# Optimization experiments

Hardware: AMD Instinct MI355X
Metric: run time of the kernel (lower is better)

## Reference

```python
import jax, jax.numpy as jnp
import numpy as np

B, S, H, E, C, V = 512, 256, 768, 6, 10, 3


def setup_inputs() -> dict:
    key = jax.random.key(0)
    ks = jax.random.split(key, 16)

    def w(k, shape):
        fan_in = shape[-1]
        return jax.random.normal(k, shape, dtype=jnp.float32) / np.sqrt(fan_in)

    return {
        'x': jax.random.randint(ks[0], (B, S), 0, V, dtype=jnp.int64),
        'emb': w(ks[1], (V, E)),
        'W_fx': w(ks[2], (H, E)), 'W_fh': w(ks[3], (H, H)), 'b_f': w(ks[4], (H, 1)),
        'W_ix': w(ks[5], (H, E)), 'W_ih': w(ks[6], (H, H)), 'b_i': w(ks[7], (H, 1)),
        'W_ox': w(ks[8], (H, E)), 'W_oh': w(ks[9], (H, H)), 'b_o': w(ks[10], (H, 1)),
        'W_cx': w(ks[11], (H, E)), 'b_c': w(ks[12], (H, 1)),
        'W_ph': w(ks[13], (C, H)), 'b_p': w(ks[14], (C, 1)),
        'c_init': jax.random.normal(ks[15], (H, B), dtype=jnp.float32) / np.sqrt(B),
    }


def reference(x, emb, W_fx, W_fh, b_f, W_ix, W_ih, b_i, W_ox, W_oh, b_o,
              W_cx, b_c, W_ph, b_p, c_init):
    # Embed tokens: [B, S] -> [B, S, E] -> time-major [S, E, B]
    xe = jnp.transpose(emb[x], (1, 2, 0))
    xs = xe[: S - 1]  # loop runs seq_length - 1 steps

    def step(carry, x_t):
        c_prev, _ = carry  # c_prev: [H, B], x_t: [E, B]
        f_t = jax.nn.sigmoid(W_fx @ x_t + W_fh @ c_prev + b_f)
        i_t = jax.nn.sigmoid(W_ix @ x_t + W_ih @ c_prev + b_i)
        o_t = jax.nn.sigmoid(W_ox @ x_t + W_oh @ c_prev + b_o)
        c_t = jax.nn.sigmoid(W_cx @ x_t + b_c) * i_t + c_prev * f_t
        h_t = jnp.tanh(c_t) * o_t
        return (c_t, h_t), None

    h0 = jnp.zeros((H, B), dtype=c_init.dtype)
    (c_fin, h_fin), _ = jax.lax.scan(step, (c_init, h0), xs)
    p_t = W_ph @ h_fin + b_p  # [C, B]
    return jax.nn.log_softmax(p_t.T, axis=-1)  # [B, C]
```

## Files before the change

kernel.cpp:

```cpp
#include <hip/hip_runtime.h>


typedef _Float16 f16x8 __attribute__((ext_vector_type(8)));
typedef _Float16 f16x4 __attribute__((ext_vector_type(4)));
typedef float    f32x4 __attribute__((ext_vector_type(4)));

#define Hdim  768
#define Bdim  512
#define Sdim  256
#define NSTEP 255
#define Edim  6
#define NCls  10
#define NGRP  16
#define NRB   12
#define GC    32
#define HB    64
#define NKK   24
#define CSTR  776
#define XSTR  260
#define PLANE (Bdim * Hdim)
#define SCL      4096.0f
#define SCL_INV  2.44140625e-4f

#define WP_FRAGS   (2 * NRB * 4 * NKK * 64)
#define WS_CBUF    0u
#define WS_HFIN    (2u * 2u * PLANE * 2u)
#define WS_BAR     (WS_HFIN + Bdim * Hdim * 4u)
#define WS_WPK     (WS_BAR + 4096u)
#define WS_BAR_BYTES (NGRP * 16u * 4u)

__device__ __forceinline__ float sigf(float z) { return 1.0f / (1.0f + __expf(-z)); }

__device__ __forceinline__ f32x4 mf(f16x8 a, f16x8 b, f32x4 c) {
    return __builtin_amdgcn_mfma_f32_16x16x32_f16(a, b, c, 0, 0, 0);
}

__global__ void __launch_bounds__(256)
prep_w(const float* __restrict__ Wfh, const float* __restrict__ Wih,
       _Float16* __restrict__ wpk)
{
    const int fid  = blockIdx.x * 256 + threadIdx.x;
    const int lane = fid & 63;
    const int t1   = fid >> 6;
    const int kk   = t1 % NKK;
    const int gi   = t1 / NKK;
    const int sub  = gi & 3;
    const int t3   = gi >> 2;
    const int rb   = t3 % NRB;
    const int gate = t3 / NRB;
    const int q = lane >> 4, r = lane & 15;
    const int row = rb * 64 + sub * 16 + r;
    const int col = kk * 32 + q * 8;
    const float* src = (gate ? Wih : Wfh) + (size_t)row * Hdim + col;
    f16x8 hi, lo;
    #pragma unroll
    for (int j = 0; j < 8; ++j) {
        const float v = src[j];
        const _Float16 h = (_Float16)v;
        hi[j] = h;
        lo[j] = (_Float16)((v - (float)h) * SCL);
    }
    *(f16x8*)&wpk[(size_t)fid * 8] = hi;
    *(f16x8*)&wpk[((size_t)WP_FRAGS + fid) * 8] = lo;
}

__global__ void __launch_bounds__(512, 1)
lstm_persist(const int* __restrict__ xk, const float* __restrict__ emb,
             const float* __restrict__ Wfx, const float* __restrict__ bfv,
             const float* __restrict__ Wix, const float* __restrict__ biv,
             const float* __restrict__ Wox, const float* __restrict__ Woh,
             const float* __restrict__ bov,
             const float* __restrict__ Wcx, const float* __restrict__ bcv,
             const float* __restrict__ cinit,
             const _Float16* __restrict__ wpk,
             _Float16* __restrict__ cbuf, float* __restrict__ hfin,
             unsigned int* __restrict__ bar)
{
    __shared__ __align__(16) _Float16 ldsH[GC * CSTR];
    __shared__ __align__(16) _Float16 ldsM[GC * CSTR];
    __shared__ __align__(16) float    tbl[3 * HB * 4];
    __shared__ __align__(16) float    zbuf[HB * GC];
    __shared__ __align__(4)  unsigned char xtok[GC * XSTR];
    __shared__ int s_flag;
    __shared__ unsigned int fdone;

    const int tid  = threadIdx.x;
    const int w    = tid >> 6;
    const int lane = tid & 63;
    const int q    = lane >> 4;
    const int r    = lane & 15;
    const int gt   = w >> 2;
    const int sub  = w & 3;
    const int bid  = blockIdx.x;
    const int g    = bid & 15;
    const int rb   = bid >> 4;
    const int blkh0 = rb * HB;
    const int gc0   = g * GC;
    const int hq0   = blkh0 + sub * 16 + q * 4;
    const int gi    = (gt * NRB + rb) * 4 + sub;

    if (tid == 0) { s_flag = 0; fdone = 0u; }
    __syncthreads();
    if (tid < 256) {
        if (xk[(size_t)gc0 * Sdim + 2 * tid + 1] != 0) s_flag = 1;
    }
    if (tid < 3 * HB) {
        const int v  = tid >> 6;
        const int hl = tid & 63;
        const int hg = blkh0 + hl;
        float pf = bfv[hg], pi = biv[hg], po = bov[hg], pc = bcv[hg];
        #pragma unroll
        for (int e = 0; e < Edim; ++e) {
            const float ev = emb[v * Edim + e];
            pf += Wfx[hg * Edim + e] * ev;
            pi += Wix[hg * Edim + e] * ev;
            po += Wox[hg * Edim + e] * ev;
            pc += Wcx[hg * Edim + e] * ev;
        }
        float* t = &tbl[(v * HB + hl) * 4];
        t[0] = pf; t[1] = pi; t[2] = po; t[3] = sigf(pc);
    }
    __syncthreads();
    const int is64 = (s_flag == 0);

    {
        const int col   = tid >> 4;
        const int sbase = (tid & 15) * 16;
        const size_t rowb = (size_t)(gc0 + col) * Sdim;
        for (int k2 = 0; k2 < 16; ++k2) {
            const int s0 = sbase + k2;
            const size_t idx = rowb + s0;
            xtok[col * XSTR + s0] = (unsigned char)xk[is64 ? (idx << 1) : idx];
        }
    }

    f16x8 whi[NKK], wlo[NKK];
    #pragma unroll
    for (int kk = 0; kk < NKK; ++kk) {
        whi[kk] = *(const f16x8*)&wpk[((size_t)(gi * NKK + kk) * 64 + lane) * 8];
        wlo[kk] = *(const f16x8*)&wpk[((size_t)WP_FRAGS + (size_t)(gi * NKK + kk) * 64 + lane) * 8];
    }

    float cst[2][4];
    #pragma unroll
    for (int ct = 0; ct < 2; ++ct) {
        const int b = gc0 + ct * 16 + r;
        #pragma unroll
        for (int reg = 0; reg < 4; ++reg)
            cst[ct][reg] = cinit[(size_t)(hq0 + reg) * Bdim + b];
    }

    for (int i = 0; i < 48; ++i) {
        const int idx = tid + i * 512;
        const int col = idx & 31, k = idx >> 5;
        const float v = cinit[(size_t)k * Bdim + gc0 + col];
        const _Float16 h = (_Float16)v;
        ldsH[col * CSTR + k] = h;
        ldsM[col * CSTR + k] = (_Float16)((v - (float)h) * SCL);
    }

    for (int s = 0; s < NSTEP; ++s) {
        __syncthreads();

        f32x4 a0h = {0,0,0,0}, a0x = {0,0,0,0}, a1h = {0,0,0,0}, a1x = {0,0,0,0};
        #pragma unroll
        for (int kk = 0; kk < NKK; ++kk) {
            const int lo = kk * 32 + q * 8;
            const f16x8 bh0 = *(const f16x8*)&ldsH[ r       * CSTR + lo];
            const f16x8 bm0 = *(const f16x8*)&ldsM[ r       * CSTR + lo];
            const f16x8 bh1 = *(const f16x8*)&ldsH[(16 + r) * CSTR + lo];
            const f16x8 bm1 = *(const f16x8*)&ldsM[(16 + r) * CSTR + lo];
            a0h = mf(whi[kk], bh0, a0h);
            a0x = mf(whi[kk], bm0, a0x);
            a0x = mf(wlo[kk], bh0, a0x);
            a1h = mf(whi[kk], bh1, a1h);
            a1x = mf(whi[kk], bm1, a1x);
            a1x = mf(wlo[kk], bh1, a1x);
        }
        if (gt) {
            #pragma unroll
            for (int ct = 0; ct < 2; ++ct) {
                const f32x4 zh = ct ? a1h : a0h;
                const f32x4 zx = ct ? a1x : a0x;
                #pragma unroll
                for (int reg = 0; reg < 4; ++reg)
                    zbuf[(sub * 16 + q * 4 + reg) * GC + ct * 16 + r] =
                        zh[reg] + zx[reg] * SCL_INV;
            }
        }
        __syncthreads();

        if (!gt) {
            if (s != NSTEP - 1) {
                _Float16* cwH = cbuf + (size_t)(((s + 1) & 1) * 2) * PLANE;
                _Float16* cwM = cwH + PLANE;
                #pragma unroll
                for (int ct = 0; ct < 2; ++ct) {
                    const int bl = ct * 16 + r;
                    const int v  = xtok[bl * XSTR + s];
                    const float* tb = &tbl[(v * HB + sub * 16 + q * 4) * 4];
                    const f32x4 zh = ct ? a1h : a0h;
                    const f32x4 zx = ct ? a1x : a0x;
                    f16x4 cvh, cvm;
                    #pragma unroll
                    for (int reg = 0; reg < 4; ++reg) {
                        const float zf = zh[reg] + zx[reg] * SCL_INV;
                        const float zi = zbuf[(sub * 16 + q * 4 + reg) * GC + bl];
                        const float* tt = tb + reg * 4;
                        const float fg = sigf(zf + tt[0]);
                        const float ig = sigf(zi + tt[1]);
                        const float cn = tt[3] * ig + cst[ct][reg] * fg;
                        cst[ct][reg] = cn;
                        const _Float16 ch = (_Float16)cn;
                        cvh[reg] = ch;
                        cvm[reg] = (_Float16)((cn - (float)ch) * SCL);
                    }
                    unsigned long long uh, um;
                    __builtin_memcpy(&uh, &cvh, 8);
                    __builtin_memcpy(&um, &cvm, 8);
                    const size_t eo = (size_t)(gc0 + bl) * Hdim + hq0;
                    __hip_atomic_store((unsigned long long*)&cwH[eo], uh,
                                       __ATOMIC_RELAXED, __HIP_MEMORY_SCOPE_AGENT);
                    __hip_atomic_store((unsigned long long*)&cwM[eo], um,
                                       __ATOMIC_RELAXED, __HIP_MEMORY_SCOPE_AGENT);
                }
                asm volatile("s_waitcnt vmcnt(0)" ::: "memory");
                if (lane == 0) {
                    const unsigned old = __hip_atomic_fetch_add(&fdone, 1u,
                                         __ATOMIC_ACQ_REL, __HIP_MEMORY_SCOPE_WORKGROUP);
                    if (old == 4u * (unsigned)s + 3u)
                        __hip_atomic_store(&bar[g * 16 + rb], (unsigned)(s + 1),
                                           __ATOMIC_RELAXED, __HIP_MEMORY_SCOPE_AGENT);
                }
            } else {
                f32x4 o0h = {0,0,0,0}, o0x = {0,0,0,0}, o1h = {0,0,0,0}, o1x = {0,0,0,0};
                const int arow = blkh0 + sub * 16 + r;
                #pragma unroll
                for (int kk = 0; kk < NKK; ++kk) {
                    const float* wp = Woh + (size_t)arow * Hdim + kk * 32 + q * 8;
                    f16x8 who;
                    #pragma unroll
                    for (int j = 0; j < 8; ++j) who[j] = (_Float16)wp[j];
                    const int lo = kk * 32 + q * 8;
                    const f16x8 bh0 = *(const f16x8*)&ldsH[ r       * CSTR + lo];
                    const f16x8 bm0 = *(const f16x8*)&ldsM[ r       * CSTR + lo];
                    const f16x8 bh1 = *(const f16x8*)&ldsH[(16 + r) * CSTR + lo];
                    const f16x8 bm1 = *(const f16x8*)&ldsM[(16 + r) * CSTR + lo];
                    o0h = mf(who, bh0, o0h);  o0x = mf(who, bm0, o0x);
                    o1h = mf(who, bh1, o1h);  o1x = mf(who, bm1, o1x);
                }
                #pragma unroll
                for (int ct = 0; ct < 2; ++ct) {
                    const int bl = ct * 16 + r;
                    const int v  = xtok[bl * XSTR + s];
                    const float* tb = &tbl[(v * HB + sub * 16 + q * 4) * 4];
                    const f32x4 zh = ct ? a1h : a0h;
                    const f32x4 zx = ct ? a1x : a0x;
                    const f32x4 zoh = ct ? o1h : o0h;
                    const f32x4 zox = ct ? o1x : o0x;
                    f32x4 hv;
                    #pragma unroll
                    for (int reg = 0; reg < 4; ++reg) {
                        const float zf = zh[reg] + zx[reg] * SCL_INV;
                        const float zi = zbuf[(sub * 16 + q * 4 + reg) * GC + bl];
                        const float zo = zoh[reg] + zox[reg] * SCL_INV;
                        const float* tt = tb + reg * 4;
                        const float fg = sigf(zf + tt[0]);
                        const float ig = sigf(zi + tt[1]);
                        const float og = sigf(zo + tt[2]);
                        const float cn = tt[3] * ig + cst[ct][reg] * fg;
                        const float e  = __expf(-2.0f * fabsf(cn));
                        const float th = __builtin_copysignf((1.0f - e) / (1.0f + e), cn);
                        hv[reg] = th * og;
                    }
                    *(f32x4*)&hfin[(size_t)(gc0 + bl) * Hdim + hq0] = hv;
                }
            }
        }

        if (s < NSTEP - 1) {
            const unsigned tgt = (unsigned)(s + 1);
            while (true) {
                unsigned vv = tgt;
                if (lane < NRB)
                    vv = __hip_atomic_load(&bar[g * 16 + lane],
                                           __ATOMIC_RELAXED, __HIP_MEMORY_SCOPE_AGENT);
                if (__all(vv >= tgt)) break;
                __builtin_amdgcn_s_sleep(1);
            }
            const _Float16* crH = cbuf + (size_t)(((s + 1) & 1) * 2) * PLANE;
            const _Float16* crM = crH + PLANE;
            const int col = tid >> 4, j = tid & 15;
            const size_t rowo = (size_t)(gc0 + col) * Hdim;
            {
                unsigned long long th[12];
                #pragma unroll
                for (int i = 0; i < 12; ++i)
                    th[i] = __hip_atomic_load((unsigned long long*)&crH[rowo + (j + 16 * i) * 4],
                                              __ATOMIC_RELAXED, __HIP_MEMORY_SCOPE_AGENT);
                #pragma unroll
                for (int i = 0; i < 12; ++i)
                    *(unsigned long long*)&ldsH[col * CSTR + (j + 16 * i) * 4] = th[i];
            }
            {
                unsigned long long tm[12];
                #pragma unroll
                for (int i = 0; i < 12; ++i)
                    tm[i] = __hip_atomic_load((unsigned long long*)&crM[rowo + (j + 16 * i) * 4],
                                              __ATOMIC_RELAXED, __HIP_MEMORY_SCOPE_AGENT);
                #pragma unroll
                for (int i = 0; i < 12; ++i)
                    *(unsigned long long*)&ldsM[col * CSTR + (j + 16 * i) * 4] = tm[i];
            }
        }
    }
}

__global__ void __launch_bounds__(64)
proj_kernel(const float* __restrict__ hfin, const float* __restrict__ Wph,
            const float* __restrict__ bpv, float* __restrict__ out)
{
    const int b = blockIdx.x;
    const int lane = threadIdx.x;
    float acc[NCls];
    #pragma unroll
    for (int c = 0; c < NCls; ++c) acc[c] = 0.f;
    const float* hb = &hfin[(size_t)b * Hdim];
    for (int i = 0; i < Hdim / 64; ++i) {
        const float hv = hb[lane + i * 64];
        #pragma unroll
        for (int c = 0; c < NCls; ++c)
            acc[c] += Wph[c * Hdim + lane + i * 64] * hv;
    }
    #pragma unroll
    for (int c = 0; c < NCls; ++c) {
        float v = acc[c];
        #pragma unroll
        for (int off = 32; off > 0; off >>= 1)
            v += __shfl_xor(v, off, 64);
        acc[c] = v + bpv[c];
    }
    float m = acc[0];
    #pragma unroll
    for (int c = 1; c < NCls; ++c) m = fmaxf(m, acc[c]);
    float ssum = 0.f;
    #pragma unroll
    for (int c = 0; c < NCls; ++c) ssum += __expf(acc[c] - m);
    const float lse = m + __logf(ssum);
    if (lane < NCls) out[b * NCls + lane] = acc[lane] - lse;
}

extern "C" void kernel_launch(void* const* d_in, const int* in_sizes, int n_in,
                              void* d_out, int out_size, void* d_ws, size_t ws_size,
                              hipStream_t stream)
{
    const int*   xk    = (const int*)d_in[0];
    const float* emb   = (const float*)d_in[1];
    const float* Wfx   = (const float*)d_in[2];
    const float* Wfh   = (const float*)d_in[3];
    const float* bfv   = (const float*)d_in[4];
    const float* Wix   = (const float*)d_in[5];
    const float* Wih   = (const float*)d_in[6];
    const float* biv   = (const float*)d_in[7];
    const float* Wox   = (const float*)d_in[8];
    const float* Woh   = (const float*)d_in[9];
    const float* bov   = (const float*)d_in[10];
    const float* Wcx   = (const float*)d_in[11];
    const float* bcv   = (const float*)d_in[12];
    const float* Wph   = (const float*)d_in[13];
    const float* bpv   = (const float*)d_in[14];
    const float* cinit = (const float*)d_in[15];

    char* ws = (char*)d_ws;
    _Float16*     cbuf = (_Float16*)(ws + WS_CBUF);
    float*        hfin = (float*)(ws + WS_HFIN);
    unsigned int* bar  = (unsigned int*)(ws + WS_BAR);
    _Float16*     wpk  = (_Float16*)(ws + WS_WPK);

    hipMemsetAsync(bar, 0, WS_BAR_BYTES, stream);

    prep_w<<<dim3(WP_FRAGS / 256), dim3(256), 0, stream>>>(Wfh, Wih, wpk);

    lstm_persist<<<dim3(NGRP * NRB), dim3(512), 0, stream>>>(
        xk, emb, Wfx, bfv, Wix, biv, Wox, Woh, bov, Wcx, bcv,
        cinit, wpk, cbuf, hfin, bar);

    proj_kernel<<<dim3(Bdim), dim3(64), 0, stream>>>(hfin, Wph, bpv, (float*)d_out);
}
```

Measured before the change: 2.582 ms.

## Add dedicated loader warps with per-chunk LDS flags to overlap state fetch with MFMA

Raises the block to 768 threads so four extra warps become producers. They poll each row-block's global barrier flag on its own and copy that chunk of the fp16 hi/lo state into LDS, then release per-chunk ready counters. The eight compute warps start MFMAs on each K-chunk as soon as it lands, which replaces the block-wide syncthreads and the all-rows barrier wait. zbuf is double-buffered and handed off through an LDS counter. The cost is more spin-waiting on LDS atomics and extra register pressure from the larger block, which keepalive asm is used to pin weights in registers.

```diff
diff --git a/kernel.cpp b/kernel.cpp
--- a/kernel.cpp
+++ b/kernel.cpp
@@ -4,6 +4,7 @@
 typedef _Float16 f16x8 __attribute__((ext_vector_type(8)));
 typedef _Float16 f16x4 __attribute__((ext_vector_type(4)));
 typedef float    f32x4 __attribute__((ext_vector_type(4)));
+typedef unsigned long long u64;
 
 #define Hdim  768
 #define Bdim  512
@@ -16,6 +17,7 @@
 #define GC    32
 #define HB    64
 #define NKK   24
+#define NCH   12
 #define CSTR  776
 #define XSTR  260
 #define PLANE (Bdim * Hdim)
@@ -33,6 +35,10 @@
 
 __device__ __forceinline__ f32x4 mf(f16x8 a, f16x8 b, f32x4 c) {
     return __builtin_amdgcn_mfma_f32_16x16x32_f16(a, b, c, 0, 0, 0);
+}
+
+__device__ __forceinline__ void keepalive(f16x8& x) {
+    asm volatile("" : "+v"(x));
 }
 
 __global__ void __launch_bounds__(256)
@@ -64,7 +70,7 @@
     *(f16x8*)&wpk[((size_t)WP_FRAGS + fid) * 8] = lo;
 }
 
-__global__ void __launch_bounds__(512, 1)
+__global__ void __launch_bounds__(768, 1)
 lstm_persist(const int* __restrict__ xk, const float* __restrict__ emb,
              const float* __restrict__ Wfx, const float* __restrict__ bfv,
              const float* __restrict__ Wix, const float* __restrict__ biv,
@@ -79,27 +85,29 @@
     __shared__ __align__(16) _Float16 ldsH[GC * CSTR];
     __shared__ __align__(16) _Float16 ldsM[GC * CSTR];
     __shared__ __align__(16) float    tbl[3 * HB * 4];
-    __shared__ __align__(16) float    zbuf[HB * GC];
+    __shared__ __align__(16) float    zbuf[2][HB * GC];
     __shared__ __align__(4)  unsigned char xtok[GC * XSTR];
+    __shared__ unsigned int ldsRdy[NCH];
+    __shared__ unsigned int chunkDone[NCH];
+    __shared__ unsigned int zdone, fdone;
     __shared__ int s_flag;
-    __shared__ unsigned int fdone;
 
     const int tid  = threadIdx.x;
     const int w    = tid >> 6;
     const int lane = tid & 63;
     const int q    = lane >> 4;
     const int r    = lane & 15;
-    const int gt   = w >> 2;
-    const int sub  = w & 3;
     const int bid  = blockIdx.x;
     const int g    = bid & 15;
     const int rb   = bid >> 4;
     const int blkh0 = rb * HB;
     const int gc0   = g * GC;
-    const int hq0   = blkh0 + sub * 16 + q * 4;
-    const int gi    = (gt * NRB + rb) * 4 + sub;
-
-    if (tid == 0) { s_flag = 0; fdone = 0u; }
+
+    if (tid == 0) {
+        s_flag = 0; zdone = 0u; fdone = 0u;
+        #pragma unroll
+        for (int j = 0; j < NCH; ++j) { ldsRdy[j] = 0u; chunkDone[j] = 0u; }
+    }
     __syncthreads();
     if (tid < 256) {
         if (xk[(size_t)gc0 * Sdim + 2 * tid + 1] != 0) s_flag = 1;
@@ -123,7 +131,7 @@
     __syncthreads();
     const int is64 = (s_flag == 0);
 
-    {
+    if (tid < 512) {
         const int col   = tid >> 4;
         const int sbase = (tid & 15) * 16;
         const size_t rowb = (size_t)(gc0 + col) * Sdim;
@@ -134,183 +142,209 @@
         }
     }
 
-    f16x8 whi[NKK], wlo[NKK];
-    #pragma unroll
-    for (int kk = 0; kk < NKK; ++kk) {
-        whi[kk] = *(const f16x8*)&wpk[((size_t)(gi * NKK + kk) * 64 + lane) * 8];
-        wlo[kk] = *(const f16x8*)&wpk[((size_t)WP_FRAGS + (size_t)(gi * NKK + kk) * 64 + lane) * 8];
-    }
-
-    float cst[2][4];
-    #pragma unroll
-    for (int ct = 0; ct < 2; ++ct) {
-        const int b = gc0 + ct * 16 + r;
-        #pragma unroll
-        for (int reg = 0; reg < 4; ++reg)
-            cst[ct][reg] = cinit[(size_t)(hq0 + reg) * Bdim + b];
-    }
-
-    for (int i = 0; i < 48; ++i) {
-        const int idx = tid + i * 512;
+    for (int i = 0; i < 32; ++i) {
+        const int idx = tid + i * 768;
         const int col = idx & 31, k = idx >> 5;
         const float v = cinit[(size_t)k * Bdim + gc0 + col];
         const _Float16 h = (_Float16)v;
         ldsH[col * CSTR + k] = h;
         ldsM[col * CSTR + k] = (_Float16)((v - (float)h) * SCL);
     }
-
-    for (int s = 0; s < NSTEP; ++s) {
-        __syncthreads();
-
-        f32x4 a0h = {0,0,0,0}, a0x = {0,0,0,0}, a1h = {0,0,0,0}, a1x = {0,0,0,0};
+    __syncthreads();
+
+    if (w < 8) {
+        const int gt  = w >> 2;
+        const int sub = w & 3;
+        const int hq0 = blkh0 + sub * 16 + q * 4;
+        const int gi  = (gt * NRB + rb) * 4 + sub;
+
+        f16x8 whi[NKK], wlo[NKK];
         #pragma unroll
         for (int kk = 0; kk < NKK; ++kk) {
-            const int lo = kk * 32 + q * 8;
-            const f16x8 bh0 = *(const f16x8*)&ldsH[ r       * CSTR + lo];
-            const f16x8 bm0 = *(const f16x8*)&ldsM[ r       * CSTR + lo];
-            const f16x8 bh1 = *(const f16x8*)&ldsH[(16 + r) * CSTR + lo];
-            const f16x8 bm1 = *(const f16x8*)&ldsM[(16 + r) * CSTR + lo];
-            a0h = mf(whi[kk], bh0, a0h);
-            a0x = mf(whi[kk], bm0, a0x);
-            a0x = mf(wlo[kk], bh0, a0x);
-            a1h = mf(whi[kk], bh1, a1h);
-            a1x = mf(whi[kk], bm1, a1x);
-            a1x = mf(wlo[kk], bh1, a1x);
-        }
-        if (gt) {
+            whi[kk] = *(const f16x8*)&wpk[((size_t)(gi * NKK + kk) * 64 + lane) * 8];
+            wlo[kk] = *(const f16x8*)&wpk[((size_t)WP_FRAGS + (size_t)(gi * NKK + kk) * 64 + lane) * 8];
+        }
+        #pragma unroll
+        for (int kk = 0; kk < NKK; ++kk) { keepalive(whi[kk]); keepalive(wlo[kk]); }
+
+        float cst[2][4];
+        #pragma unroll
+        for (int ct = 0; ct < 2; ++ct) {
+            const int b = gc0 + ct * 16 + r;
             #pragma unroll
-            for (int ct = 0; ct < 2; ++ct) {
-                const f32x4 zh = ct ? a1h : a0h;
-                const f32x4 zx = ct ? a1x : a0x;
+            for (int reg = 0; reg < 4; ++reg)
+                cst[ct][reg] = cinit[(size_t)(hq0 + reg) * Bdim + b];
+        }
+
+        for (int s = 0; s < NSTEP; ++s) {
+            f32x4 a0h = {0,0,0,0}, a0x = {0,0,0,0}, a1h = {0,0,0,0}, a1x = {0,0,0,0};
+            const unsigned rdyTgt = 4u * (unsigned)s;
+            for (int j = 0; j < NCH; ++j) {
+                while (__hip_atomic_load(&ldsRdy[j], __ATOMIC_ACQUIRE,
+                                         __HIP_MEMORY_SCOPE_WORKGROUP) < rdyTgt)
+                    __builtin_amdgcn_s_sleep(1);
                 #pragma unroll
-                for (int reg = 0; reg < 4; ++reg)
-                    zbuf[(sub * 16 + q * 4 + reg) * GC + ct * 16 + r] =
-                        zh[reg] + zx[reg] * SCL_INV;
-            }
-        }
-        __syncthreads();
-
-        if (!gt) {
-            if (s != NSTEP - 1) {
-                _Float16* cwH = cbuf + (size_t)(((s + 1) & 1) * 2) * PLANE;
-                _Float16* cwM = cwH + PLANE;
-                #pragma unroll
-                for (int ct = 0; ct < 2; ++ct) {
-                    const int bl = ct * 16 + r;
-                    const int v  = xtok[bl * XSTR + s];
-                    const float* tb = &tbl[(v * HB + sub * 16 + q * 4) * 4];
-                    const f32x4 zh = ct ? a1h : a0h;
-                    const f32x4 zx = ct ? a1x : a0x;
-                    f16x4 cvh, cvm;
-                    #pragma unroll
-                    for (int reg = 0; reg < 4; ++reg) {
-                        const float zf = zh[reg] + zx[reg] * SCL_INV;
-                        const float zi = zbuf[(sub * 16 + q * 4 + reg) * GC + bl];
-                        const float* tt = tb + reg * 4;
-                        const float fg = sigf(zf + tt[0]);
-                        const float ig = sigf(zi + tt[1]);
-                        const float cn = tt[3] * ig + cst[ct][reg] * fg;
-                        cst[ct][reg] = cn;
-                        const _Float16 ch = (_Float16)cn;
-                        cvh[reg] = ch;
-                        cvm[reg] = (_Float16)((cn - (float)ch) * SCL);
-                    }
-                    unsigned long long uh, um;
-                    __builtin_memcpy(&uh, &cvh, 8);
-                    __builtin_memcpy(&um, &cvm, 8);
-                    const size_t eo = (size_t)(gc0 + bl) * Hdim + hq0;
-                    __hip_atomic_store((unsigned long long*)&cwH[eo], uh,
-                                       __ATOMIC_RELAXED, __HIP_MEMORY_SCOPE_AGENT);
-                    __hip_atomic_store((unsigned long long*)&cwM[eo], um,
-                                       __ATOMIC_RELAXED, __HIP_MEMORY_SCOPE_AGENT);
-                }
-                asm volatile("s_waitcnt vmcnt(0)" ::: "memory");
-                if (lane == 0) {
-                    const unsigned old = __hip_atomic_fetch_add(&fdone, 1u,
-                                         __ATOMIC_ACQ_REL, __HIP_MEMORY_SCOPE_WORKGROUP);
-                    if (old == 4u * (unsigned)s + 3u)
-                        __hip_atomic_store(&bar[g * 16 + rb], (unsigned)(s + 1),
-                                           __ATOMIC_RELAXED, __HIP_MEMORY_SCOPE_AGENT);
-                }
-            } else {
-                f32x4 o0h = {0,0,0,0}, o0x = {0,0,0,0}, o1h = {0,0,0,0}, o1x = {0,0,0,0};
-                const int arow = blkh0 + sub * 16 + r;
-                #pragma unroll
-                for (int kk = 0; kk < NKK; ++kk) {
-                    const float* wp = Woh + (size_t)arow * Hdim + kk * 32 + q * 8;
-                    f16x8 who;
-                    #pragma unroll
-                    for (int j = 0; j < 8; ++j) who[j] = (_Float16)wp[j];
+                for (int k2 = 0; k2 < 2; ++k2) {
+                    const int kk = j * 2 + k2;
                     const int lo = kk * 32 + q * 8;
                     const f16x8 bh0 = *(const f16x8*)&ldsH[ r       * CSTR + lo];
                     const f16x8 bm0 = *(const f16x8*)&ldsM[ r       * CSTR + lo];
                     const f16x8 bh1 = *(const f16x8*)&ldsH[(16 + r) * CSTR + lo];
                     const f16x8 bm1 = *(const f16x8*)&ldsM[(16 + r) * CSTR + lo];
-                    o0h = mf(who, bh0, o0h);  o0x = mf(who, bm0, o0x);
-                    o1h = mf(who, bh1, o1h);  o1x = mf(who, bm1, o1x);
+                    a0h = mf(whi[kk], bh0, a0h);
+                    a0x = mf(whi[kk], bm0, a0x);
+                    a0x = mf(wlo[kk], bh0, a0x);
+                    a1h = mf(whi[kk], bh1, a1h);
+                    a1x = mf(whi[kk], bm1, a1x);
+                    a1x = mf(wlo[kk], bh1, a1x);
                 }
+                if (lane == 0)
+                    __hip_atomic_fetch_add(&chunkDone[j], 1u, __ATOMIC_RELEASE,
+                                           __HIP_MEMORY_SCOPE_WORKGROUP);
+            }
+
+            if (gt) {
+                float* zp = zbuf[s & 1];
                 #pragma unroll
                 for (int ct = 0; ct < 2; ++ct) {
-                    const int bl = ct * 16 + r;
-                    const int v  = xtok[bl * XSTR + s];
-                    const float* tb = &tbl[(v * HB + sub * 16 + q * 4) * 4];
                     const f32x4 zh = ct ? a1h : a0h;
                     const f32x4 zx = ct ? a1x : a0x;
-                    const f32x4 zoh = ct ? o1h : o0h;
-                    const f32x4 zox = ct ? o1x : o0x;
-                    f32x4 hv;
                     #pragma unroll
-                    for (int reg = 0; reg < 4; ++reg) {
-                        const float zf = zh[reg] + zx[reg] * SCL_INV;
-                        const float zi = zbuf[(sub * 16 + q * 4 + reg) * GC + bl];
-                        const float zo = zoh[reg] + zox[reg] * SCL_INV;
-                        const float* tt = tb + reg * 4;
-                        const float fg = sigf(zf + tt[0]);
-                        const float ig = sigf(zi + tt[1]);
-                        const float og = sigf(zo + tt[2]);
-                        const float cn = tt[3] * ig + cst[ct][reg] * fg;
-                        const float e  = __expf(-2.0f * fabsf(cn));
-                        const float th = __builtin_copysignf((1.0f - e) / (1.0f + e), cn);
-                        hv[reg] = th * og;
+                    for (int reg = 0; reg < 4; ++reg)
+                        zp[(sub * 16 + q * 4 + reg) * GC + ct * 16 + r] =
+                            zh[reg] + zx[reg] * SCL_INV;
+                }
+                if (lane == 0)
+                    __hip_atomic_fetch_add(&zdone, 1u, __ATOMIC_RELEASE,
+                                           __HIP_MEMORY_SCOPE_WORKGROUP);
+            } else {
+                const unsigned zTgt = 4u * (unsigned)(s + 1);
+                while (__hip_atomic_load(&zdone, __ATOMIC_ACQUIRE,
+                                         __HIP_MEMORY_SCOPE_WORKGROUP) < zTgt)
+                    __builtin_amdgcn_s_sleep(1);
+                const float* zp = zbuf[s & 1];
+
+                if (s != NSTEP - 1) {
+                    _Float16* cwH = cbuf + (size_t)(((s + 1) & 1) * 2) * PLANE;
+                    _Float16* cwM = cwH + PLANE;
+                    #pragma unroll
+                    for (int ct = 0; ct < 2; ++ct) {
+                        const int bl = ct * 16 + r;
+                        const int v  = xtok[bl * XSTR + s];
+                        const float* tb = &tbl[(v * HB + sub * 16 + q * 4) * 4];
+                        const f32x4 zh = ct ? a1h : a0h;
+                        const f32x4 zx = ct ? a1x : a0x;
+                        f16x4 cvh, cvm;
+                        #pragma unroll
+                        for (int reg = 0; reg < 4; ++reg) {
+                            const float zf = zh[reg] + zx[reg] * SCL_INV;
+                            const float zi = zp[(sub * 16 + q * 4 + reg) * GC + bl];
+                            const float* tt = tb + reg * 4;
+                            const float fg = sigf(zf + tt[0]);
+                            const float ig = sigf(zi + tt[1]);
+                            const float cn = tt[3] * ig + cst[ct][reg] * fg;
+                            cst[ct][reg] = cn;
+                            const _Float16 ch = (_Float16)cn;
+                            cvh[reg] = ch;
+                            cvm[reg] = (_Float16)((cn - (float)ch) * SCL);
+                        }
+                        u64 uh, um;
+                        __builtin_memcpy(&uh, &cvh, 8);
+                        __builtin_memcpy(&um, &cvm, 8);
+                        const size_t eo = (size_t)(gc0 + bl) * Hdim + hq0;
+                        __hip_atomic_store((u64*)&cwH[eo], uh,
+                                           __ATOMIC_RELAXED, __HIP_MEMORY_SCOPE_AGENT);
+                        __hip_atomic_store((u64*)&cwM[eo], um,
+                                           __ATOMIC_RELAXED, __HIP_MEMORY_SCOPE_AGENT);
                     }
-                    *(f32x4*)&hfin[(size_t)(gc0 + bl) * Hdim + hq0] = hv;
+                    asm volatile("s_waitcnt vmcnt(0)" ::: "memory");
+                    if (lane == 0) {
+                        const unsigned old = __hip_atomic_fetch_add(&fdone, 1u,
+                                             __ATOMIC_ACQ_REL, __HIP_MEMORY_SCOPE_WORKGROUP);
+                        if (old == 4u * (unsigned)s + 3u)
+                            __hip_atomic_store(&bar[g * 16 + rb], (unsigned)(s + 1),
+                                               __ATOMIC_RELAXED, __HIP_MEMORY_SCOPE_AGENT);
+                    }
+                } else {
+                    f32x4 o0h = {0,0,0,0}, o0x = {0,0,0,0}, o1h = {0,0,0,0}, o1x = {0,0,0,0};
+                    const int arow = blkh0 + sub * 16 + r;
+                    #pragma unroll
+                    for (int kk = 0; kk < NKK; ++kk) {
+                        const float* wp = Woh + (size_t)arow * Hdim + kk * 32 + q * 8;
+                        f16x8 who;
+                        #pragma unroll
+                        for (int jj = 0; jj < 8; ++jj) who[jj] = (_Float16)wp[jj];
+                        const int lo = kk * 32 + q * 8;
+                        const f16x8 bh0 = *(const f16x8*)&ldsH[ r       * CSTR + lo];
+                        const f16x8 bm0 = *(const f16x8*)&ldsM[ r       * CSTR + lo];
+                        const f16x8 bh1 = *(const f16x8*)&ldsH[(16 + r) * CSTR + lo];
+                        const f16x8 bm1 = *(const f16x8*)&ldsM[(16 + r) * CSTR + lo];
+                        o0h = mf(who, bh0, o0h);  o0x = mf(who, bm0, o0x);
+                        o1h = mf(who, bh1, o1h);  o1x = mf(who, bm1, o1x);
+                    }
+                    #pragma unroll
+                    for (int ct = 0; ct < 2; ++ct) {
+                        const int bl = ct * 16 + r;
+                        const int v  = xtok[bl * XSTR + s];
+                        const float* tb = &tbl[(v * HB + sub * 16 + q * 4) * 4];
+                        const f32x4 zh = ct ? a1h : a0h;
+                        const f32x4 zx = ct ? a1x : a0x;
+                        const f32x4 zoh = ct ? o1h : o0h;
+                        const f32x4 zox = ct ? o1x : o0x;
+                        f32x4 hv;
+                        #pragma unroll
+                        for (int reg = 0; reg < 4; ++reg) {
+                            const float zf = zh[reg] + zx[reg] * SCL_INV;
+                            const float zi = zp[(sub * 16 + q * 4 + reg) * GC + bl];
+                            const float zo = zoh[reg] + zox[reg] * SCL_INV;
+                            const float* tt = tb + reg * 4;
+                            const float fg = sigf(zf + tt[0]);
+                            const float ig = sigf(zi + tt[1]);
+                            const float og = sigf(zo + tt[2]);
+                            const float cn = tt[3] * ig + cst[ct][reg] * fg;
+                            const float e  = __expf(-2.0f * fabsf(cn));
+                            const float th = __builtin_copysignf((1.0f - e) / (1.0f + e), cn);
+                            hv[reg] = th * og;
+                        }
+                        *(f32x4*)&hfin[(size_t)(gc0 + bl) * Hdim + hq0] = hv;
+                    }
                 }
             }
         }
-
-        if (s < NSTEP - 1) {
-            const unsigned tgt = (unsigned)(s + 1);
-            while (true) {
-                unsigned vv = tgt;
-                if (lane < NRB)
-                    vv = __hip_atomic_load(&bar[g * 16 + lane],
-                                           __ATOMIC_RELAXED, __HIP_MEMORY_SCOPE_AGENT);
-                if (__all(vv >= tgt)) break;
-                __builtin_amdgcn_s_sleep(1);
+    } else {
+        const int sw   = w - 8;
+        const int slot = sw * 64 + lane;
+        const int p    = slot >> 7;
+        const int colq = (slot >> 2) & 31;
+        const int seg  = slot & 3;
+        _Float16* ldsP = p ? ldsM : ldsH;
+        const size_t rowo = (size_t)(gc0 + colq) * Hdim;
+
+        for (int s = 1; s < NSTEP; ++s) {
+            const _Float16* cr = cbuf + (size_t)((s & 1) * 2 + p) * PLANE + rowo;
+            u64 d[NCH][4];
+            #pragma unroll
+            for (int j = 0; j < NCH; ++j) {
+                while (__hip_atomic_load(&bar[g * 16 + j], __ATOMIC_RELAXED,
+                                         __HIP_MEMORY_SCOPE_AGENT) < (unsigned)s)
+                    __builtin_amdgcn_s_sleep(2);
+                const size_t ko = (size_t)j * 64 + seg * 16;
+                #pragma unroll
+                for (int t = 0; t < 4; ++t)
+                    d[j][t] = __hip_atomic_load((const u64*)&cr[ko + 4 * t],
+                                                __ATOMIC_RELAXED, __HIP_MEMORY_SCOPE_AGENT);
             }
-            const _Float16* crH = cbuf + (size_t)(((s + 1) & 1) * 2) * PLANE;
-            const _Float16* crM = crH + PLANE;
-            const int col = tid >> 4, j = tid & 15;
-            const size_t rowo = (size_t)(gc0 + col) * Hdim;
-            {
-                unsigned long long th[12];
-                #pragma unroll
-                for (int i = 0; i < 12; ++i)
-                    th[i] = __hip_atomic_load((unsigned long long*)&crH[rowo + (j + 16 * i) * 4],
-                                              __ATOMIC_RELAXED, __HIP_MEMORY_SCOPE_AGENT);
-                #pragma unroll
-                for (int i = 0; i < 12; ++i)
-                    *(unsigned long long*)&ldsH[col * CSTR + (j + 16 * i) * 4] = th[i];
-            }
-            {
-                unsigned long long tm[12];
-                #pragma unroll
-                for (int i = 0; i < 12; ++i)
-                    tm[i] = __hip_atomic_load((unsigned long long*)&crM[rowo + (j + 16 * i) * 4],
-                                              __ATOMIC_RELAXED, __HIP_MEMORY_SCOPE_AGENT);
-                #pragma unroll
-                for (int i = 0; i < 12; ++i)
-                    *(unsigned long long*)&ldsM[col * CSTR + (j + 16 * i) * 4] = tm[i];
+            const unsigned doneTgt = 8u * (unsigned)s;
+            #pragma unroll
+            for (int j = 0; j < NCH; ++j) {
+                while (__hip_atomic_load(&chunkDone[j], __ATOMIC_ACQUIRE,
+                                         __HIP_MEMORY_SCOPE_WORKGROUP) < doneTgt)
+                    __builtin_amdgcn_s_sleep(1);
+                u64* dst = (u64*)&ldsP[colq * CSTR + j * 64 + seg * 16];
+                dst[0] = d[j][0]; dst[1] = d[j][1]; dst[2] = d[j][2]; dst[3] = d[j][3];
+                if (lane == 0)
+                    __hip_atomic_fetch_add(&ldsRdy[j], 1u, __ATOMIC_RELEASE,
+                                           __HIP_MEMORY_SCOPE_WORKGROUP);
             }
         }
     }
@@ -381,7 +415,7 @@
 
     prep_w<<<dim3(WP_FRAGS / 256), dim3(256), 0, stream>>>(Wfh, Wih, wpk);
 
-    lstm_persist<<<dim3(NGRP * NRB), dim3(512), 0, stream>>>(
+    lstm_persist<<<dim3(NGRP * NRB), dim3(768), 0, stream>>>(
         xk, emb, Wfx, bfv, Wix, biv, Wox, Woh, bov, Wcx, bcv,
         cinit, wpk, cbuf, hfin, bar);
 
```

Measured after the change: 5.172 ms. 2x slower.
